# Kernel optimization log

Hardware: AMD Instinct MI355X
Metric: run time of the kernel (lower is better)

The kernel has to match this reference:

```python
import jax, jax.numpy as jnp
import numpy as np

N = 50000      # nodes
E = 600000     # edges
F_ATOM = 78
D = 128        # hidden_dim = heads * head_dim
H = 8
C = D // H     # 16
ED = 12        # edge_dim
L = 4          # num_layers
B = 512        # graphs in batch
DFF = 4 * D
SCALE = 1.0 / float(np.sqrt(C))


def setup_inputs() -> dict:
    key = jax.random.key(0)
    ks = iter(jax.random.split(key, 128))
    rn = lambda s, sc=0.05: jax.random.normal(next(ks), s, jnp.float32) * sc
    inp = {
        "x": jax.random.normal(next(ks), (N, F_ATOM), jnp.float32),
        "edge_attr": jax.random.normal(next(ks), (E, ED), jnp.float32),
        "edge_index": jax.random.randint(next(ks), (2, E), 0, N),
        "batch": jnp.sort(jax.random.randint(next(ks), (N,), 0, B)),
        "Wemb": rn((F_ATOM, D)), "bemb": jnp.zeros((D,), jnp.float32),
        "Wout": rn((D, D)), "bout": jnp.zeros((D,), jnp.float32),
    }
    def stk(s, sc=0.05):
        return jnp.stack([rn(s, sc) for _ in range(L)])
    inp.update(
        Wq=stk((D, D)), bq=jnp.zeros((L, D), jnp.float32),
        Wk=stk((D, D)), bk=jnp.zeros((L, D), jnp.float32),
        Wv=stk((D, D)), bv=jnp.zeros((L, D), jnp.float32),
        We=stk((ED, D)), be=jnp.zeros((L, D), jnp.float32),
        Wskip=stk((D, D)), bskip=jnp.zeros((L, D), jnp.float32),
        Wbeta=stk((3 * D,)),
        g1=jnp.ones((L, D), jnp.float32), b1=jnp.zeros((L, D), jnp.float32),
        g2=jnp.ones((L, D), jnp.float32), b2=jnp.zeros((L, D), jnp.float32),
        Wf1=stk((D, DFF)), bf1=jnp.zeros((L, DFF), jnp.float32),
        Wf2=stk((DFF, D)), bf2=jnp.zeros((L, D), jnp.float32),
    )
    return inp


def _ln(x, g, b):
    mu = jnp.mean(x, -1, keepdims=True)
    var = jnp.mean((x - mu) ** 2, -1, keepdims=True)
    return (x - mu) * jax.lax.rsqrt(var + 1e-5) * g + b


def _seg_softmax(alpha, dst):
    # alpha: [E, H]; softmax over edges sharing a destination node
    m = jax.ops.segment_max(alpha, dst, num_segments=N)
    m = jnp.where(jnp.isfinite(m), m, 0.0)
    ex = jnp.exp(alpha - m[dst])
    den = jax.ops.segment_sum(ex, dst, num_segments=N)
    return ex / (den[dst] + 1e-16)


def _forward(x, edge_attr, Wemb, bemb, Wq, bq, Wk, bk, Wv, bv, We, be,
             Wskip, bskip, Wbeta, g1, b1, g2, b2, Wf1, bf1, Wf2, bf2,
             Wout, bout, edge_index, batch):
    src, dst = edge_index[0], edge_index[1]
    h = x @ Wemb + bemb                                    # [N, D]
    for l in range(L):
        q = (h @ Wq[l] + bq[l]).reshape(N, H, C)
        k = (h @ Wk[l] + bk[l]).reshape(N, H, C)
        v = (h @ Wv[l] + bv[l]).reshape(N, H, C)
        e = (edge_attr @ We[l] + be[l]).reshape(E, H, C)
        kj = k[src] + e                                    # [E, H, C]
        alpha = jnp.einsum('ehc,ehc->eh', q[dst], kj) * SCALE
        a = _seg_softmax(alpha, dst)                       # [E, H]
        msg = (v[src] + e) * a[:, :, None]                 # [E, H, C]
        agg = jax.ops.segment_sum(msg, dst, num_segments=N).reshape(N, D)
        xr = h @ Wskip[l] + bskip[l]                       # root/skip transform
        beta = jax.nn.sigmoid(
            jnp.concatenate([agg, xr, agg - xr], -1) @ Wbeta[l])[:, None]
        hc = beta * xr + (1.0 - beta) * agg                # beta gate
        h = _ln(hc + h, g1[l], b1[l])
        ff = jax.nn.relu(h @ Wf1[l] + bf1[l]) @ Wf2[l] + bf2[l]
        h = _ln(ff + h, g2[l], b2[l])
    cnt = jax.ops.segment_sum(jnp.ones((N,), h.dtype), batch, num_segments=B)
    pooled = jax.ops.segment_sum(h, batch, num_segments=B) / jnp.maximum(cnt, 1.0)[:, None]
    return pooled @ Wout + bout                            # [B, D]


def reference(x, edge_attr, edge_index, batch, Wemb, bemb, Wout, bout,
              Wq, bq, Wk, bk, Wv, bv, We, be, Wskip, bskip, Wbeta,
              g1, b1, g2, b2, Wf1, bf1, Wf2, bf2):
    return _forward(x, edge_attr, Wemb, bemb, Wq, bq, Wk, bk, Wv, bv, We, be,
                    Wskip, bskip, Wbeta, g1, b1, g2, b2, Wf1, bf1, Wf2, bf2,
                    Wout, bout, edge_index, batch)
```

## Files before the change

kernel.cpp:

```cpp
#include <hip/hip_runtime.h>
#include <math.h>

#define N_NODES 50000
#define N_EDGES 600000
#define FATOM   78
#define DIM     128
#define HEADS   8
#define EDIM    12
#define LAYERS  4
#define NBATCH  512
#define NDFF    512
#define ASCALE  0.25f

typedef __attribute__((ext_vector_type(8))) short bf16x8;
typedef __attribute__((ext_vector_type(4))) float f32x4;

__device__ __forceinline__ float sum16(float v){
  #pragma unroll
  for (int m=1;m<16;m<<=1) v += __shfl_xor(v, m);
  return v;
}
__device__ __forceinline__ short f2b(float f){
  unsigned int u = __builtin_bit_cast(unsigned int, f);
  u += 0x7fffu + ((u>>16)&1u);
  return (short)(u>>16);
}
__device__ __forceinline__ float b2f_lo(unsigned int u){ return __builtin_bit_cast(float, u<<16); }
__device__ __forceinline__ float b2f_hi(unsigned int u){ return __builtin_bit_cast(float, u & 0xffff0000u); }

__device__ __forceinline__ void gload16(const short* g, short* l){
  __builtin_amdgcn_global_load_lds(
      (const __attribute__((address_space(1))) void*)g,
      (__attribute__((address_space(3))) void*)l, 16, 0, 0);
}

__global__ void count_kernel(const int* __restrict__ ei, int* __restrict__ cnt){
  int e = blockIdx.x*256 + threadIdx.x;
  if (e < N_EDGES) atomicAdd(&cnt[ei[N_EDGES + e]], 1);
}

__global__ __launch_bounds__(1024) void scan1(const int* __restrict__ cnt,
                                              int* __restrict__ row_start, int* __restrict__ bsum){
  __shared__ int lds[1024];
  int gid = blockIdx.x*1024 + threadIdx.x;
  int v = (gid < N_NODES) ? cnt[gid] : 0;
  lds[threadIdx.x] = v; __syncthreads();
  for (int off=1; off<1024; off<<=1){
    int add = (threadIdx.x>=off)?lds[threadIdx.x-off]:0;
    __syncthreads();
    lds[threadIdx.x]+=add;
    __syncthreads();
  }
  if (gid < N_NODES) row_start[gid+1] = lds[threadIdx.x];
  if (threadIdx.x==1023) bsum[blockIdx.x] = lds[1023];
}
__global__ void scan2(int* __restrict__ bsum, int nb){
  int tid = threadIdx.x;
  int v = (tid < nb) ? bsum[tid] : 0;
  #pragma unroll
  for (int off=1; off<64; off<<=1){
    int u = __shfl_up(v, off);
    if (tid >= off) v += u;
  }
  if (tid < nb) bsum[tid] = v;
}
__global__ void scan3(int* __restrict__ row_start, const int* __restrict__ bsum){
  int gid = blockIdx.x*256 + threadIdx.x;
  if (gid == 0) row_start[0] = 0;
  if (gid < N_NODES){
    int blk = gid >> 10;
    if (blk > 0) row_start[gid+1] += bsum[blk-1];
  }
}

__global__ void scatter_kernel(const int* __restrict__ ei, const float* __restrict__ ea,
                               int* __restrict__ cnt2, const int* __restrict__ row_start,
                               int* __restrict__ src_s, short* __restrict__ ea_s){
  int e = blockIdx.x*256 + threadIdx.x;
  if (e < N_EDGES){
    int d = ei[N_EDGES + e];
    int pos = atomicAdd(&cnt2[d], 1);
    int p = row_start[d] + pos;
    src_s[p] = ei[e];
    const float* src = ea + (size_t)e*EDIM;
    unsigned int* dst = (unsigned int*)(ea_s + (size_t)p*EDIM);
    #pragma unroll
    for (int j=0;j<6;j++){
      unsigned int lo = (unsigned int)(unsigned short)f2b(src[2*j]);
      unsigned int hi = (unsigned int)(unsigned short)f2b(src[2*j+1]);
      dst[j] = lo | (hi<<16);
    }
  }
}

__global__ __launch_bounds__(256) void deg_hist(const int* __restrict__ cnt, int* __restrict__ dhist){
  __shared__ int lh[256];
  lh[threadIdx.x] = 0; __syncthreads();
  int n = blockIdx.x*256 + threadIdx.x;
  if (n < N_NODES){
    int d = cnt[n]; if (d > 255) d = 255;
    atomicAdd(&lh[d], 1);
  }
  __syncthreads();
  int c = lh[threadIdx.x];
  if (c) atomicAdd(&dhist[threadIdx.x], c);
}
__global__ __launch_bounds__(256) void deg_scan(const int* __restrict__ dhist, int* __restrict__ dstart){
  __shared__ int l[256];
  int t = threadIdx.x;
  int v = dhist[t];
  l[t] = v; __syncthreads();
  for (int off=1; off<256; off<<=1){
    int add = (t>=off)? l[t-off]:0;
    __syncthreads();
    l[t]+=add;
    __syncthreads();
  }
  dstart[t] = l[t]-v;
}
__global__ __launch_bounds__(256) void deg_place(const int* __restrict__ cnt, int* __restrict__ dcnt,
                                                 const int* __restrict__ dstart, int* __restrict__ perm){
  __shared__ int lh[256];
  __shared__ int lbase[256];
  __shared__ int lrank[256];
  int t = threadIdx.x;
  lh[t] = 0; lrank[t] = 0; __syncthreads();
  int n = blockIdx.x*256 + t;
  int d = -1;
  if (n < N_NODES){
    d = cnt[n]; if (d > 255) d = 255;
    atomicAdd(&lh[d], 1);
  }
  __syncthreads();
  int c = lh[t];
  lbase[t] = c ? atomicAdd(&dcnt[t], c) : 0;
  __syncthreads();
  if (n < N_NODES){
    int r = atomicAdd(&lrank[d], 1);
    perm[dstart[d] + lbase[d] + r] = n;
  }
}

__global__ __launch_bounds__(256) void pack_weights(
  const float* __restrict__ Wq, const float* __restrict__ Wk,
  const float* __restrict__ Wv, const float* __restrict__ Ws,
  const float* __restrict__ bq, const float* __restrict__ bk,
  const float* __restrict__ bv, const float* __restrict__ bs,
  const float* __restrict__ Wf1, const float* __restrict__ Wf2,
  short* __restrict__ wq_t, short* __restrict__ wf1_t, short* __restrict__ wf2_t,
  float* __restrict__ bqkvs)
{
  int l = blockIdx.y;
  int idx = blockIdx.x*256 + threadIdx.x;
  int sec = idx >> 16, r = idx & 65535;
  if (sec == 0){
    int n = r >> 7, k = r & 127;
    const float* W = (n<128)?Wq:(n<256)?Wk:(n<384)?Wv:Ws;
    float v = W[(size_t)l*16384 + k*128 + (n&127)];
    wq_t[(size_t)l*65536 + n*128 + k] = f2b(v);
    if (k == 0){
      const float* bb = (n<128)?bq:(n<256)?bk:(n<384)?bv:bs;
      bqkvs[l*512 + n] = bb[l*128 + (n&127)];
    }
  } else if (sec == 1){
    int n = r >> 7, k = r & 127;
    wf1_t[(size_t)l*65536 + n*128 + k] = f2b(Wf1[(size_t)l*65536 + k*512 + n]);
  } else {
    int n = r >> 9, k = r & 511;
    wf2_t[(size_t)l*65536 + n*512 + k] = f2b(Wf2[(size_t)l*65536 + k*128 + n]);
  }
}

__global__ void pack_emb(const float* __restrict__ Wemb, short* __restrict__ wemb_t){
  int idx = blockIdx.x*256 + threadIdx.x;
  int nn = idx >> 7, k = idx & 127;
  wemb_t[nn*128 + k] = (k < FATOM) ? f2b(Wemb[(size_t)k*DIM + nn]) : (short)0;
}

__global__ void cast_pad_x(const float* __restrict__ x, short* __restrict__ xb){
  int idx = blockIdx.x*256 + threadIdx.x;
  int n = idx >> 6, kp = (idx & 63)*2;
  if (n >= N_NODES) return;
  float v0 = (kp   < FATOM) ? x[(size_t)n*FATOM + kp]   : 0.f;
  float v1 = (kp+1 < FATOM) ? x[(size_t)n*FATOM + kp+1] : 0.f;
  unsigned int lo = (unsigned int)(unsigned short)f2b(v0);
  unsigned int hi = (unsigned int)(unsigned short)f2b(v1);
  *(unsigned int*)(xb + (size_t)n*128 + kp) = lo | (hi<<16);
}

__global__ __launch_bounds__(256) void gemm_k128(
    const short* __restrict__ A,
    const short* __restrict__ Bt,
    const float* __restrict__ bias,
    float* __restrict__ Cf,
    short* __restrict__ Cb,
    int Nrows, int M, int relu, int nbn)
{
  __shared__ short As[128*128];
  __shared__ short Bs[128*128];
  int tid  = threadIdx.x;
  int lane = tid & 63;
  int wave = tid >> 6;
  int wr = wave >> 1, wc = wave & 1;
  int bm = blockIdx.x * 128;
  int d  = lane & 15;
  int lr = lane >> 4;

  #pragma unroll
  for (int it=0; it<8; ++it){
    int r = wave*32 + it*4 + lr;
    int oct = (d & 8) | ((d & 7) ^ (r & 7));
    int gr = bm + r; if (gr >= Nrows) gr = Nrows-1;
    gload16(A + (size_t)gr*128 + oct*8, As + (wave*32 + it*4)*128);
  }

  for (int t=0; t<nbn; ++t){
    int bn = (blockIdx.y*nbn + t)*128;
    if (t) __syncthreads();
    #pragma unroll
    for (int it=0; it<8; ++it){
      int r = wave*32 + it*4 + lr;
      int oct = (d & 8) | ((d & 7) ^ (r & 7));
      gload16(Bt + (size_t)(bn + r)*128 + oct*8, Bs + (wave*32 + it*4)*128);
    }
    f32x4 zero = {0.f,0.f,0.f,0.f};
    f32x4 acc[4][4];
    #pragma unroll
    for (int m=0;m<4;m++)
      #pragma unroll
      for (int n=0;n<4;n++) acc[m][n] = zero;

    __syncthreads();

    #pragma unroll
    for (int ks=0; ks<4; ++ks){
      int oi = ks*4 + (lane>>4);
      bf16x8 af[4], bfv[4];
      #pragma unroll
      for (int m=0;m<4;m++){
        int row = wr*64 + m*16 + (lane&15);
        int slot = (oi&8) | ((oi&7) ^ (row&7));
        af[m] = *(const bf16x8*)(As + row*128 + slot*8);
      }
      #pragma unroll
      for (int n=0;n<4;n++){
        int col = wc*64 + n*16 + (lane&15);
        int slot = (oi&8) | ((oi&7) ^ (col&7));
        bfv[n] = *(const bf16x8*)(Bs + col*128 + slot*8);
      }
      #pragma unroll
      for (int m=0;m<4;m++)
        #pragma unroll
        for (int n=0;n<4;n++)
          acc[m][n] = __builtin_amdgcn_mfma_f32_16x16x32_bf16(af[m], bfv[n], acc[m][n], 0, 0, 0);
    }

    #pragma unroll
    for (int m=0;m<4;m++){
      #pragma unroll
      for (int n=0;n<4;n++){
        int col = bn + wc*64 + n*16 + (lane&15);
        float bval = bias[col];
        #pragma unroll
        for (int j=0;j<4;j++){
          int row = bm + wr*64 + m*16 + (lane>>4)*4 + j;
          if (row < Nrows){
            float v = acc[m][n][j] + bval;
            if (relu) v = fmaxf(v, 0.f);
            if (Cf) Cf[(size_t)row*M + col] = v;
            if (Cb) Cb[(size_t)row*M + col] = f2b(v);
          }
        }
      }
    }
  }
}

__global__ __launch_bounds__(256) void gemm_ff2_ln(
    const short* __restrict__ A,
    const short* __restrict__ Bt,
    const float* __restrict__ bias,
    float* __restrict__ h, short* __restrict__ hb,
    const float* __restrict__ g, const float* __restrict__ b,
    int Nrows)
{
  __shared__ short As[128*64];
  __shared__ short Bs[128*64];
  __shared__ float red[2][128][2];
  int tid  = threadIdx.x;
  int lane = tid & 63;
  int wave = tid >> 6;
  int wr = wave >> 1, wc = wave & 1;
  int bm = blockIdx.x * 128;

  f32x4 zero = {0.f,0.f,0.f,0.f};
  f32x4 acc[4][4];
  #pragma unroll
  for (int m=0;m<4;m++)
    #pragma unroll
    for (int n=0;n<4;n++) acc[m][n] = zero;

  int r0 = wave*32;
  for (int k0 = 0; k0 < 512; k0 += 64){
    #pragma unroll
    for (int it=0; it<4; ++it){
      int rr = r0 + it*8;
      int r  = rr + (lane>>3);
      int oct = (lane&7) ^ (r&7);
      int gr = bm + r; if (gr >= Nrows) gr = Nrows-1;
      gload16(A  + (size_t)gr*512 + k0 + oct*8, As + rr*64);
      gload16(Bt + (size_t)r*512  + k0 + oct*8, Bs + rr*64);
    }
    __syncthreads();
    #pragma unroll
    for (int ks=0; ks<2; ++ks){
      bf16x8 af[4], bfv[4];
      #pragma unroll
      for (int m=0;m<4;m++){
        int row = wr*64 + m*16 + (lane&15);
        int oi  = ks*4 + (lane>>4);
        af[m] = *(const bf16x8*)(As + row*64 + ((oi ^ (row&7))<<3));
      }
      #pragma unroll
      for (int n=0;n<4;n++){
        int col = wc*64 + n*16 + (lane&15);
        int oi  = ks*4 + (lane>>4);
        bfv[n] = *(const bf16x8*)(Bs + col*64 + ((oi ^ (col&7))<<3));
      }
      #pragma unroll
      for (int m=0;m<4;m++)
        #pragma unroll
        for (int n=0;n<4;n++)
          acc[m][n] = __builtin_amdgcn_mfma_f32_16x16x32_bf16(af[m], bfv[n], acc[m][n], 0, 0, 0);
    }
    __syncthreads();
  }

  #pragma unroll
  for (int m=0;m<4;m++){
    #pragma unroll
    for (int n=0;n<4;n++){
      int col = wc*64 + n*16 + (lane&15);
      float bval = bias[col];
      #pragma unroll
      for (int j=0;j<4;j++){
        int row = wr*64 + m*16 + (lane>>4)*4 + j;
        int grow = bm + row; if (grow >= Nrows) grow = Nrows-1;
        acc[m][n][j] += bval + h[(size_t)grow*DIM + col];
      }
    }
  }
  #pragma unroll
  for (int m=0;m<4;m++){
    #pragma unroll
    for (int j=0;j<4;j++){
      float ps = 0.f, pq = 0.f;
      #pragma unroll
      for (int n=0;n<4;n++){ float v = acc[m][n][j]; ps += v; pq += v*v; }
      #pragma unroll
      for (int msk=1; msk<16; msk<<=1){ ps += __shfl_xor(ps, msk); pq += __shfl_xor(pq, msk); }
      if ((lane&15)==0){
        int row = wr*64 + m*16 + (lane>>4)*4 + j;
        red[wc][row][0] = ps;
        red[wc][row][1] = pq;
      }
    }
  }
  __syncthreads();
  #pragma unroll
  for (int m=0;m<4;m++){
    #pragma unroll
    for (int j=0;j<4;j++){
      int row = wr*64 + m*16 + (lane>>4)*4 + j;
      float S = red[0][row][0] + red[1][row][0];
      float Q = red[0][row][1] + red[1][row][1];
      float mu  = S*(1.f/128.f);
      float var = fmaxf(Q*(1.f/128.f) - mu*mu, 0.f);
      float rr  = rsqrtf(var + 1e-5f);
      int grow = bm + row;
      if (grow < Nrows){
        #pragma unroll
        for (int n=0;n<4;n++){
          int col = wc*64 + n*16 + (lane&15);
          float o = (acc[m][n][j]-mu)*rr*g[col] + b[col];
          h[(size_t)grow*DIM + col]  = o;
          hb[(size_t)grow*DIM + col] = f2b(o);
        }
      }
    }
  }
}

__global__ __launch_bounds__(256) void edge_attn_fused(
  const short* __restrict__ qkvx,
  const short* __restrict__ ea_s, const int* __restrict__ src_s,
  const float* __restrict__ Wel, const float* __restrict__ bel,
  const int* __restrict__ row_start, const int* __restrict__ perm,
  float* __restrict__ h, short* __restrict__ hb,
  const float* __restrict__ Wb, const float* __restrict__ g, const float* __restrict__ b)
{
  int wid = (blockIdx.x*256 + threadIdx.x) >> 4;
  if (wid >= N_NODES) return;
  int node = perm[wid];
  int ln = threadIdx.x & 15;
  int c0 = ln*8;

  const short* qrow = qkvx + (size_t)node*512;
  uint4 qu = *(const uint4*)(qrow + c0);
  float q0=b2f_lo(qu.x), q1=b2f_hi(qu.x), q2=b2f_lo(qu.y), q3=b2f_hi(qu.y);
  float q4=b2f_lo(qu.z), q5=b2f_hi(qu.z), q6=b2f_lo(qu.w), q7=b2f_hi(qu.w);

  float u[12];
  #pragma unroll
  for (int j=0;j<12;j++){
    float4 wA = *(const float4*)(Wel + j*DIM + c0);
    float4 wB = *(const float4*)(Wel + j*DIM + c0 + 4);
    float pp = q0*wA.x+q1*wA.y+q2*wA.z+q3*wA.w
             + q4*wB.x+q5*wB.y+q6*wB.z+q7*wB.w;
    u[j] = pp + __shfl_xor(pp,1);
  }
  float4 beA = *(const float4*)(bel + c0);
  float4 beB = *(const float4*)(bel + c0 + 4);
  float qbe;
  { float pp = q0*beA.x+q1*beA.y+q2*beA.z+q3*beA.w
             + q4*beB.x+q5*beB.y+q6*beB.z+q7*beB.w;
    qbe = pp + __shfl_xor(pp,1); }

  int rs = row_start[node], re = row_start[node+1];
  float den = 0.f;
  float av[8] = {0.f,0.f,0.f,0.f,0.f,0.f,0.f,0.f};
  float aEA[12] = {0.f,0.f,0.f,0.f,0.f,0.f,0.f,0.f,0.f,0.f,0.f,0.f};

  int i = rs;
  for (; i+2 <= re; i += 2){
    int s0 = src_s[i], s1 = src_s[i+1];
    const short* e0p = ea_s + (size_t)i*EDIM;
    uint2 a00 = *(const uint2*)(e0p);
    uint2 a01 = *(const uint2*)(e0p+4);
    uint2 a02 = *(const uint2*)(e0p+8);
    uint2 a10 = *(const uint2*)(e0p+12);
    uint2 a11 = *(const uint2*)(e0p+16);
    uint2 a12 = *(const uint2*)(e0p+20);
    const short* r0p = qkvx + (size_t)s0*512;
    const short* r1p = qkvx + (size_t)s1*512;
    uint4 ku0 = *(const uint4*)(r0p + 128 + c0);
    uint4 vu0 = *(const uint4*)(r0p + 256 + c0);
    uint4 ku1 = *(const uint4*)(r1p + 128 + c0);
    uint4 vu1 = *(const uint4*)(r1p + 256 + c0);

    float ea0[12], ea1[12];
    ea0[0]=b2f_lo(a00.x); ea0[1]=b2f_hi(a00.x); ea0[2]=b2f_lo(a00.y); ea0[3]=b2f_hi(a00.y);
    ea0[4]=b2f_lo(a01.x); ea0[5]=b2f_hi(a01.x); ea0[6]=b2f_lo(a01.y); ea0[7]=b2f_hi(a01.y);
    ea0[8]=b2f_lo(a02.x); ea0[9]=b2f_hi(a02.x); ea0[10]=b2f_lo(a02.y); ea0[11]=b2f_hi(a02.y);
    ea1[0]=b2f_lo(a10.x); ea1[1]=b2f_hi(a10.x); ea1[2]=b2f_lo(a10.y); ea1[3]=b2f_hi(a10.y);
    ea1[4]=b2f_lo(a11.x); ea1[5]=b2f_hi(a11.x); ea1[6]=b2f_lo(a11.y); ea1[7]=b2f_hi(a11.y);
    ea1[8]=b2f_lo(a12.x); ea1[9]=b2f_hi(a12.x); ea1[10]=b2f_lo(a12.y); ea1[11]=b2f_hi(a12.y);

    float pp0 = q0*b2f_lo(ku0.x) + q1*b2f_hi(ku0.x) + q2*b2f_lo(ku0.y) + q3*b2f_hi(ku0.y)
              + q4*b2f_lo(ku0.z) + q5*b2f_hi(ku0.z) + q6*b2f_lo(ku0.w) + q7*b2f_hi(ku0.w);
    float pp1 = q0*b2f_lo(ku1.x) + q1*b2f_hi(ku1.x) + q2*b2f_lo(ku1.y) + q3*b2f_hi(ku1.y)
              + q4*b2f_lo(ku1.z) + q5*b2f_hi(ku1.z) + q6*b2f_lo(ku1.w) + q7*b2f_hi(ku1.w);
    float al0 = pp0 + __shfl_xor(pp0,1) + qbe;
    float al1 = pp1 + __shfl_xor(pp1,1) + qbe;
    #pragma unroll
    for (int j=0;j<12;j++){ al0 += ea0[j]*u[j]; al1 += ea1[j]*u[j]; }
    float p0 = __expf(al0 * ASCALE);
    float p1 = __expf(al1 * ASCALE);
    den += p0 + p1;
    av[0] += p0*b2f_lo(vu0.x) + p1*b2f_lo(vu1.x);
    av[1] += p0*b2f_hi(vu0.x) + p1*b2f_hi(vu1.x);
    av[2] += p0*b2f_lo(vu0.y) + p1*b2f_lo(vu1.y);
    av[3] += p0*b2f_hi(vu0.y) + p1*b2f_hi(vu1.y);
    av[4] += p0*b2f_lo(vu0.z) + p1*b2f_lo(vu1.z);
    av[5] += p0*b2f_hi(vu0.z) + p1*b2f_hi(vu1.z);
    av[6] += p0*b2f_lo(vu0.w) + p1*b2f_lo(vu1.w);
    av[7] += p0*b2f_hi(vu0.w) + p1*b2f_hi(vu1.w);
    #pragma unroll
    for (int j=0;j<12;j++) aEA[j] += p0*ea0[j] + p1*ea1[j];
  }
  if (i < re){
    int s = src_s[i];
    const short* eap = ea_s + (size_t)i*EDIM;
    uint2 eu0 = *(const uint2*)(eap);
    uint2 eu1 = *(const uint2*)(eap+4);
    uint2 eu2 = *(const uint2*)(eap+8);
    float ea0[12];
    ea0[0]=b2f_lo(eu0.x); ea0[1]=b2f_hi(eu0.x); ea0[2]=b2f_lo(eu0.y); ea0[3]=b2f_hi(eu0.y);
    ea0[4]=b2f_lo(eu1.x); ea0[5]=b2f_hi(eu1.x); ea0[6]=b2f_lo(eu1.y); ea0[7]=b2f_hi(eu1.y);
    ea0[8]=b2f_lo(eu2.x); ea0[9]=b2f_hi(eu2.x); ea0[10]=b2f_lo(eu2.y); ea0[11]=b2f_hi(eu2.y);
    const short* srow = qkvx + (size_t)s*512;
    uint4 ku = *(const uint4*)(srow + 128 + c0);
    uint4 vu = *(const uint4*)(srow + 256 + c0);
    float pp = q0*b2f_lo(ku.x) + q1*b2f_hi(ku.x) + q2*b2f_lo(ku.y) + q3*b2f_hi(ku.y)
             + q4*b2f_lo(ku.z) + q5*b2f_hi(ku.z) + q6*b2f_lo(ku.w) + q7*b2f_hi(ku.w);
    float alpha = pp + __shfl_xor(pp,1) + qbe;
    #pragma unroll
    for (int j=0;j<12;j++) alpha += ea0[j]*u[j];
    float p = __expf(alpha * ASCALE);
    den += p;
    av[0] += p*b2f_lo(vu.x); av[1] += p*b2f_hi(vu.x);
    av[2] += p*b2f_lo(vu.y); av[3] += p*b2f_hi(vu.y);
    av[4] += p*b2f_lo(vu.z); av[5] += p*b2f_hi(vu.z);
    av[6] += p*b2f_lo(vu.w); av[7] += p*b2f_hi(vu.w);
    #pragma unroll
    for (int j=0;j<12;j++) aEA[j] += p*ea0[j];
  }

  float inv = 1.f/(den + 1e-16f);
  float gg[8];
  #pragma unroll
  for (int c=0;c<8;c++) gg[c] = av[c]*inv;
  #pragma unroll
  for (int j=0;j<12;j++){
    float wgt = aEA[j]*inv;
    float4 wA = *(const float4*)(Wel + j*DIM + c0);
    float4 wB = *(const float4*)(Wel + j*DIM + c0 + 4);
    gg[0]+=wgt*wA.x; gg[1]+=wgt*wA.y; gg[2]+=wgt*wA.z; gg[3]+=wgt*wA.w;
    gg[4]+=wgt*wB.x; gg[5]+=wgt*wB.y; gg[6]+=wgt*wB.z; gg[7]+=wgt*wB.w;
  }
  if (re > rs){
    gg[0]+=beA.x; gg[1]+=beA.y; gg[2]+=beA.z; gg[3]+=beA.w;
    gg[4]+=beB.x; gg[5]+=beB.y; gg[6]+=beB.z; gg[7]+=beB.w;
  }

  uint4 xu = *(const uint4*)(qrow + 384 + c0);
  float x[8];
  x[0]=b2f_lo(xu.x); x[1]=b2f_hi(xu.x); x[2]=b2f_lo(xu.y); x[3]=b2f_hi(xu.y);
  x[4]=b2f_lo(xu.z); x[5]=b2f_hi(xu.z); x[6]=b2f_lo(xu.w); x[7]=b2f_hi(xu.w);
  float4 hA = *(const float4*)(h + (size_t)node*DIM + c0);
  float4 hB = *(const float4*)(h + (size_t)node*DIM + c0 + 4);
  float hv[8] = {hA.x,hA.y,hA.z,hA.w,hB.x,hB.y,hB.z,hB.w};
  float4 waA = *(const float4*)(Wb + c0),       waB = *(const float4*)(Wb + c0 + 4);
  float4 wxA = *(const float4*)(Wb + DIM + c0), wxB = *(const float4*)(Wb + DIM + c0 + 4);
  float4 wdA = *(const float4*)(Wb + 2*DIM + c0), wdB = *(const float4*)(Wb + 2*DIM + c0 + 4);
  float wa[8] = {waA.x,waA.y,waA.z,waA.w,waB.x,waB.y,waB.z,waB.w};
  float wx[8] = {wxA.x,wxA.y,wxA.z,wxA.w,wxB.x,wxB.y,wxB.z,wxB.w};
  float wd[8] = {wdA.x,wdA.y,wdA.z,wdA.w,wdB.x,wdB.y,wdB.z,wdB.w};
  float sacc = 0.f;
  #pragma unroll
  for (int c=0;c<8;c++) sacc += gg[c]*wa[c] + x[c]*wx[c] + (gg[c]-x[c])*wd[c];
  sacc = sum16(sacc);
  float beta = 1.f/(1.f + __expf(-sacc));
  float t[8], ts = 0.f;
  #pragma unroll
  for (int c=0;c<8;c++){ t[c] = beta*x[c] + (1.f-beta)*gg[c] + hv[c]; ts += t[c]; }
  float mu = sum16(ts)*(1.f/128.f);
  float vs = 0.f;
  #pragma unroll
  for (int c=0;c<8;c++){ t[c] -= mu; vs += t[c]*t[c]; }
  float var = sum16(vs)*(1.f/128.f);
  float r = rsqrtf(var + 1e-5f);
  float4 gA = *(const float4*)(g + c0), gB = *(const float4*)(g + c0 + 4);
  float4 bA = *(const float4*)(b + c0), bB = *(const float4*)(b + c0 + 4);
  float gv[8] = {gA.x,gA.y,gA.z,gA.w,gB.x,gB.y,gB.z,gB.w};
  float bv[8] = {bA.x,bA.y,bA.z,bA.w,bB.x,bB.y,bB.z,bB.w};
  float o[8];
  #pragma unroll
  for (int c=0;c<8;c++) o[c] = t[c]*r*gv[c] + bv[c];
  float4 oA = {o[0],o[1],o[2],o[3]}, oB = {o[4],o[5],o[6],o[7]};
  *(float4*)(h + (size_t)node*DIM + c0)     = oA;
  *(float4*)(h + (size_t)node*DIM + c0 + 4) = oB;
  uint4 ou;
  ou.x = (unsigned int)(unsigned short)f2b(o[0]) | ((unsigned int)(unsigned short)f2b(o[1])<<16);
  ou.y = (unsigned int)(unsigned short)f2b(o[2]) | ((unsigned int)(unsigned short)f2b(o[3])<<16);
  ou.z = (unsigned int)(unsigned short)f2b(o[4]) | ((unsigned int)(unsigned short)f2b(o[5])<<16);
  ou.w = (unsigned int)(unsigned short)f2b(o[6]) | ((unsigned int)(unsigned short)f2b(o[7])<<16);
  *(uint4*)(hb + (size_t)node*DIM + c0) = ou;
}

__global__ __launch_bounds__(128) void pool_out(
  const float* __restrict__ h, const int* __restrict__ batch,
  const float* __restrict__ Wout, const float* __restrict__ bout,
  float* __restrict__ out)
{
  int bidx = blockIdx.x;
  int d = threadIdx.x;
  __shared__ int seg[2];
  __shared__ float p[DIM];
  if (d < 2){
    int target = bidx + d;
    int lo = 0, hi = N_NODES;
    while (lo < hi){ int mid = (lo+hi)>>1; if (batch[mid] < target) lo = mid+1; else hi = mid; }
    seg[d] = lo;
  }
  __syncthreads();
  int lo = seg[0], hi = seg[1];
  float s = 0.f;
  for (int n=lo; n<hi; ++n) s += h[(size_t)n*DIM + d];
  float cnt = (float)(hi - lo);
  p[d] = s / fmaxf(cnt, 1.f);
  __syncthreads();
  float o = bout[d];
  #pragma unroll 8
  for (int kk=0; kk<DIM; ++kk) o += p[kk]*Wout[kk*DIM + d];
  out[bidx*DIM + d] = o;
}

extern "C" void kernel_launch(void* const* d_in, const int* in_sizes, int n_in,
                              void* d_out, int out_size, void* d_ws, size_t ws_size,
                              hipStream_t stream)
{
  const float* x     = (const float*)d_in[0];
  const float* ea    = (const float*)d_in[1];
  const int*   ei    = (const int*)d_in[2];
  const int*   batch = (const int*)d_in[3];
  const float* Wemb  = (const float*)d_in[4];
  const float* bemb  = (const float*)d_in[5];
  const float* Wout  = (const float*)d_in[6];
  const float* bout  = (const float*)d_in[7];
  const float* Wq    = (const float*)d_in[8];
  const float* bq    = (const float*)d_in[9];
  const float* Wk    = (const float*)d_in[10];
  const float* bk    = (const float*)d_in[11];
  const float* Wv    = (const float*)d_in[12];
  const float* bv    = (const float*)d_in[13];
  const float* We    = (const float*)d_in[14];
  const float* be    = (const float*)d_in[15];
  const float* Wskip = (const float*)d_in[16];
  const float* bskip = (const float*)d_in[17];
  const float* Wbeta = (const float*)d_in[18];
  const float* g1    = (const float*)d_in[19];
  const float* b1    = (const float*)d_in[20];
  const float* g2    = (const float*)d_in[21];
  const float* b2    = (const float*)d_in[22];
  const float* Wf1   = (const float*)d_in[23];
  const float* bf1   = (const float*)d_in[24];
  const float* Wf2   = (const float*)d_in[25];
  const float* bf2   = (const float*)d_in[26];
  float* out = (float*)d_out;

  float* ws     = (float*)d_ws;
  float* h      = ws;
  float* bqkvs  = h + (size_t)N_NODES*DIM;
  short* ea_s   = (short*)(bqkvs + LAYERS*512);
  short* hb     = ea_s + (size_t)N_EDGES*EDIM;
  short* region = hb + (size_t)N_NODES*DIM;
  short* xb     = region + (size_t)N_NODES*NDFF;
  short* wemb_t = xb + (size_t)N_NODES*DIM;
  short* wq_t   = wemb_t + DIM*DIM;
  short* wf1_t  = wq_t  + (size_t)LAYERS*NDFF*DIM;
  short* wf2_t  = wf1_t + (size_t)LAYERS*NDFF*DIM;
  int*   cnt       = (int*)(wf2_t + (size_t)LAYERS*NDFF*DIM);
  int*   cnt2      = cnt + N_NODES;
  int*   row_start = cnt2 + N_NODES;
  int*   bsum      = row_start + N_NODES + 1;
  int*   dhist     = bsum + 64;
  int*   dcnt      = dhist + 256;
  int*   dstart    = dcnt + 256;
  int*   node_perm = dstart + 256;
  int*   src_s     = node_perm + N_NODES;

  hipMemsetAsync(cnt,  0, N_NODES*sizeof(int), stream);
  hipMemsetAsync(cnt2, 0, N_NODES*sizeof(int), stream);
  hipMemsetAsync(dhist, 0, 512*sizeof(int), stream);

  const int NB_SCAN = (N_NODES + 1023)/1024;
  const int NB_DEG  = (N_NODES + 255)/256;
  count_kernel<<<(N_EDGES+255)/256, 256, 0, stream>>>(ei, cnt);
  scan1<<<NB_SCAN, 1024, 0, stream>>>(cnt, row_start, bsum);
  scan2<<<1, 64, 0, stream>>>(bsum, NB_SCAN);
  scan3<<<(N_NODES+255)/256, 256, 0, stream>>>(row_start, bsum);
  deg_hist<<<NB_DEG, 256, 0, stream>>>(cnt, dhist);
  deg_scan<<<1, 256, 0, stream>>>(dhist, dstart);
  deg_place<<<NB_DEG, 256, 0, stream>>>(cnt, dcnt, dstart, node_perm);
  scatter_kernel<<<(N_EDGES+255)/256, 256, 0, stream>>>(ei, ea, cnt2, row_start, src_s, ea_s);

  pack_weights<<<dim3(768, LAYERS), 256, 0, stream>>>(
      Wq, Wk, Wv, Wskip, bq, bk, bv, bskip, Wf1, Wf2, wq_t, wf1_t, wf2_t, bqkvs);
  pack_emb<<<64, 256, 0, stream>>>(Wemb, wemb_t);
  cast_pad_x<<<(N_NODES*64 + 255)/256, 256, 0, stream>>>(x, xb);

  int gM = (N_NODES + 127)/128;
  int attnBlocks = (N_NODES*16 + 255)/256;

  gemm_k128<<<dim3(gM, 1), 256, 0, stream>>>(xb, wemb_t, bemb, h, hb, N_NODES, DIM, 0, 1);

  for (int l=0; l<LAYERS; ++l){
    gemm_k128<<<dim3(gM, 2), 256, 0, stream>>>(
        hb, wq_t + (size_t)l*NDFF*DIM, bqkvs + l*512, nullptr, region,
        N_NODES, NDFF, 0, 2);

    edge_attn_fused<<<attnBlocks, 256, 0, stream>>>(
        region, ea_s, src_s, We + (size_t)l*EDIM*DIM, be + l*DIM, row_start, node_perm,
        h, hb, Wbeta + l*3*DIM, g1 + l*DIM, b1 + l*DIM);

    gemm_k128<<<dim3(gM, 2), 256, 0, stream>>>(
        hb, wf1_t + (size_t)l*NDFF*DIM, bf1 + l*NDFF, nullptr, region,
        N_NODES, NDFF, 1, 2);

    gemm_ff2_ln<<<dim3(gM, 1), 256, 0, stream>>>(
        region, wf2_t + (size_t)l*DIM*NDFF, bf2 + l*DIM, h, hb,
        g2 + l*DIM, b2 + l*DIM, N_NODES);
  }

  pool_out<<<NBATCH, 128, 0, stream>>>(h, batch, Wout, bout, out);
}
```

Before: 878.4 us.

## Fuse FFN up and down projections with LayerNorm into one kernel

Replaces the separate FF1 GEMM (writing a bf16 N×512 intermediate to global memory) and the FF2+LayerNorm GEMM with a single kernel. Each block takes 64 rows and loops over four 128-wide chunks of the hidden dimension: it computes ReLU(h·W1+b1) into shared memory and immediately accumulates that chunk times W2 into registers. This removes the global round trip of the FFN intermediate and one launch. The cost is a smaller row tile, W2 fragments read straight from global/L2 without staging, and more shared memory per block. The attention kernel also now walks the degree-sorted node permutation in reverse order, likely to start the highest-degree nodes first for better load balance.

```diff
diff --git a/kernel.cpp b/kernel.cpp
--- a/kernel.cpp
+++ b/kernel.cpp
@@ -234,17 +234,17 @@
 
     #pragma unroll
     for (int ks=0; ks<4; ++ks){
-      int oi = ks*4 + (lane>>4);
+      int oi = ks*4 + lr;
       bf16x8 af[4], bfv[4];
       #pragma unroll
       for (int m=0;m<4;m++){
-        int row = wr*64 + m*16 + (lane&15);
+        int row = wr*64 + m*16 + d;
         int slot = (oi&8) | ((oi&7) ^ (row&7));
         af[m] = *(const bf16x8*)(As + row*128 + slot*8);
       }
       #pragma unroll
       for (int n=0;n<4;n++){
-        int col = wc*64 + n*16 + (lane&15);
+        int col = wc*64 + n*16 + d;
         int slot = (oi&8) | ((oi&7) ^ (col&7));
         bfv[n] = *(const bf16x8*)(Bs + col*128 + slot*8);
       }
@@ -259,11 +259,11 @@
     for (int m=0;m<4;m++){
       #pragma unroll
       for (int n=0;n<4;n++){
-        int col = bn + wc*64 + n*16 + (lane&15);
+        int col = bn + wc*64 + n*16 + d;
         float bval = bias[col];
         #pragma unroll
         for (int j=0;j<4;j++){
-          int row = bm + wr*64 + m*16 + (lane>>4)*4 + j;
+          int row = bm + wr*64 + m*16 + lr*4 + j;
           if (row < Nrows){
             float v = acc[m][n][j] + bval;
             if (relu) v = fmaxf(v, 0.f);
@@ -276,91 +276,149 @@
   }
 }
 
-__global__ __launch_bounds__(256) void gemm_ff2_ln(
+__global__ __launch_bounds__(256) void gemm_ffn_ln(
     const short* __restrict__ A,
-    const short* __restrict__ Bt,
-    const float* __restrict__ bias,
+    const short* __restrict__ W1t,
+    const short* __restrict__ W2t,
+    const float* __restrict__ bias1,
+    const float* __restrict__ bias2,
     float* __restrict__ h, short* __restrict__ hb,
     const float* __restrict__ g, const float* __restrict__ b,
     int Nrows)
 {
-  __shared__ short As[128*64];
-  __shared__ short Bs[128*64];
-  __shared__ float red[2][128][2];
+  __shared__ short As[64*128];
+  __shared__ short Bs[128*128];
+  __shared__ short F1[64*128];
+  __shared__ float red[2][64][2];
   int tid  = threadIdx.x;
   int lane = tid & 63;
   int wave = tid >> 6;
   int wr = wave >> 1, wc = wave & 1;
-  int bm = blockIdx.x * 128;
+  int bm = blockIdx.x * 64;
+  int d  = lane & 15;
+  int lr = lane >> 4;
+
+  #pragma unroll
+  for (int it=0; it<4; ++it){
+    int rbase = wave*16 + it*4;
+    int r = rbase + lr;
+    int oct = (d & 8) | ((d & 7) ^ (r & 7));
+    int gr = bm + r; if (gr >= Nrows) gr = Nrows-1;
+    gload16(A + (size_t)gr*128 + oct*8, As + rbase*128);
+  }
 
   f32x4 zero = {0.f,0.f,0.f,0.f};
-  f32x4 acc[4][4];
-  #pragma unroll
-  for (int m=0;m<4;m++)
-    #pragma unroll
-    for (int n=0;n<4;n++) acc[m][n] = zero;
-
-  int r0 = wave*32;
-  for (int k0 = 0; k0 < 512; k0 += 64){
-    #pragma unroll
-    for (int it=0; it<4; ++it){
-      int rr = r0 + it*8;
-      int r  = rr + (lane>>3);
-      int oct = (lane&7) ^ (r&7);
-      int gr = bm + r; if (gr >= Nrows) gr = Nrows-1;
-      gload16(A  + (size_t)gr*512 + k0 + oct*8, As + rr*64);
-      gload16(Bt + (size_t)r*512  + k0 + oct*8, Bs + rr*64);
+  f32x4 acc2[2][4];
+  #pragma unroll
+  for (int m=0;m<2;m++)
+    #pragma unroll
+    for (int n=0;n<4;n++) acc2[m][n] = zero;
+
+  for (int t=0; t<4; ++t){
+    #pragma unroll
+    for (int it=0; it<8; ++it){
+      int rbase = wave*32 + it*4;
+      int r = rbase + lr;
+      int oct = (d & 8) | ((d & 7) ^ (r & 7));
+      gload16(W1t + (size_t)(t*128 + r)*128 + oct*8, Bs + rbase*128);
     }
     __syncthreads();
-    #pragma unroll
-    for (int ks=0; ks<2; ++ks){
-      bf16x8 af[4], bfv[4];
-      #pragma unroll
-      for (int m=0;m<4;m++){
-        int row = wr*64 + m*16 + (lane&15);
-        int oi  = ks*4 + (lane>>4);
-        af[m] = *(const bf16x8*)(As + row*64 + ((oi ^ (row&7))<<3));
+
+    f32x4 acc1[2][4];
+    #pragma unroll
+    for (int m=0;m<2;m++)
+      #pragma unroll
+      for (int n=0;n<4;n++) acc1[m][n] = zero;
+    #pragma unroll
+    for (int ks=0; ks<4; ++ks){
+      int oi = ks*4 + lr;
+      bf16x8 af[2], bfv[4];
+      #pragma unroll
+      for (int m=0;m<2;m++){
+        int row = wr*32 + m*16 + d;
+        int slot = (oi&8) | ((oi&7) ^ (row&7));
+        af[m] = *(const bf16x8*)(As + row*128 + slot*8);
       }
       #pragma unroll
       for (int n=0;n<4;n++){
-        int col = wc*64 + n*16 + (lane&15);
-        int oi  = ks*4 + (lane>>4);
-        bfv[n] = *(const bf16x8*)(Bs + col*64 + ((oi ^ (col&7))<<3));
-      }
-      #pragma unroll
-      for (int m=0;m<4;m++)
+        int cn = wc*64 + n*16 + d;
+        int slot = (oi&8) | ((oi&7) ^ (cn&7));
+        bfv[n] = *(const bf16x8*)(Bs + cn*128 + slot*8);
+      }
+      #pragma unroll
+      for (int m=0;m<2;m++)
         #pragma unroll
         for (int n=0;n<4;n++)
-          acc[m][n] = __builtin_amdgcn_mfma_f32_16x16x32_bf16(af[m], bfv[n], acc[m][n], 0, 0, 0);
+          acc1[m][n] = __builtin_amdgcn_mfma_f32_16x16x32_bf16(af[m], bfv[n], acc1[m][n], 0, 0, 0);
     }
     __syncthreads();
-  }
-
-  #pragma unroll
-  for (int m=0;m<4;m++){
+
+    #pragma unroll
+    for (int m=0;m<2;m++){
+      #pragma unroll
+      for (int n=0;n<4;n++){
+        int col = wc*64 + n*16 + d;
+        float bv1 = bias1[t*128 + col];
+        int oct2 = col >> 3, within = col & 7;
+        #pragma unroll
+        for (int j=0;j<4;j++){
+          int row = wr*32 + m*16 + lr*4 + j;
+          float v = fmaxf(acc1[m][n][j] + bv1, 0.f);
+          int so = (oct2 & 8) | ((oct2 & 7) ^ (row & 7));
+          F1[row*128 + so*8 + within] = f2b(v);
+        }
+      }
+    }
+    __syncthreads();
+
+    #pragma unroll
+    for (int ks=0; ks<4; ++ks){
+      int oi = ks*4 + lr;
+      bf16x8 af[2], bfv[4];
+      #pragma unroll
+      for (int m=0;m<2;m++){
+        int row = wr*32 + m*16 + d;
+        int slot = (oi&8) | ((oi&7) ^ (row&7));
+        af[m] = *(const bf16x8*)(F1 + row*128 + slot*8);
+      }
+      #pragma unroll
+      for (int n=0;n<4;n++){
+        int col = wc*64 + n*16 + d;
+        bfv[n] = *(const bf16x8*)(W2t + (size_t)col*512 + t*128 + oi*8);
+      }
+      #pragma unroll
+      for (int m=0;m<2;m++)
+        #pragma unroll
+        for (int n=0;n<4;n++)
+          acc2[m][n] = __builtin_amdgcn_mfma_f32_16x16x32_bf16(af[m], bfv[n], acc2[m][n], 0, 0, 0);
+    }
+  }
+
+  #pragma unroll
+  for (int m=0;m<2;m++){
     #pragma unroll
     for (int n=0;n<4;n++){
-      int col = wc*64 + n*16 + (lane&15);
-      float bval = bias[col];
+      int col = wc*64 + n*16 + d;
+      float bval = bias2[col];
       #pragma unroll
       for (int j=0;j<4;j++){
-        int row = wr*64 + m*16 + (lane>>4)*4 + j;
+        int row = wr*32 + m*16 + lr*4 + j;
         int grow = bm + row; if (grow >= Nrows) grow = Nrows-1;
-        acc[m][n][j] += bval + h[(size_t)grow*DIM + col];
-      }
-    }
-  }
-  #pragma unroll
-  for (int m=0;m<4;m++){
+        acc2[m][n][j] += bval + h[(size_t)grow*DIM + col];
+      }
+    }
+  }
+  #pragma unroll
+  for (int m=0;m<2;m++){
     #pragma unroll
     for (int j=0;j<4;j++){
       float ps = 0.f, pq = 0.f;
       #pragma unroll
-      for (int n=0;n<4;n++){ float v = acc[m][n][j]; ps += v; pq += v*v; }
+      for (int n=0;n<4;n++){ float v = acc2[m][n][j]; ps += v; pq += v*v; }
       #pragma unroll
       for (int msk=1; msk<16; msk<<=1){ ps += __shfl_xor(ps, msk); pq += __shfl_xor(pq, msk); }
-      if ((lane&15)==0){
-        int row = wr*64 + m*16 + (lane>>4)*4 + j;
+      if (d == 0){
+        int row = wr*32 + m*16 + lr*4 + j;
         red[wc][row][0] = ps;
         red[wc][row][1] = pq;
       }
@@ -368,10 +426,10 @@
   }
   __syncthreads();
   #pragma unroll
-  for (int m=0;m<4;m++){
+  for (int m=0;m<2;m++){
     #pragma unroll
     for (int j=0;j<4;j++){
-      int row = wr*64 + m*16 + (lane>>4)*4 + j;
+      int row = wr*32 + m*16 + lr*4 + j;
       float S = red[0][row][0] + red[1][row][0];
       float Q = red[0][row][1] + red[1][row][1];
       float mu  = S*(1.f/128.f);
@@ -381,8 +439,8 @@
       if (grow < Nrows){
         #pragma unroll
         for (int n=0;n<4;n++){
-          int col = wc*64 + n*16 + (lane&15);
-          float o = (acc[m][n][j]-mu)*rr*g[col] + b[col];
+          int col = wc*64 + n*16 + d;
+          float o = (acc2[m][n][j]-mu)*rr*g[col] + b[col];
           h[(size_t)grow*DIM + col]  = o;
           hb[(size_t)grow*DIM + col] = f2b(o);
         }
@@ -401,7 +459,7 @@
 {
   int wid = (blockIdx.x*256 + threadIdx.x) >> 4;
   if (wid >= N_NODES) return;
-  int node = perm[wid];
+  int node = perm[N_NODES - 1 - wid];
   int ln = threadIdx.x & 15;
   int c0 = ln*8;
 
@@ -670,7 +728,8 @@
   pack_emb<<<64, 256, 0, stream>>>(Wemb, wemb_t);
   cast_pad_x<<<(N_NODES*64 + 255)/256, 256, 0, stream>>>(x, xb);
 
-  int gM = (N_NODES + 127)/128;
+  int gM  = (N_NODES + 127)/128;
+  int gM64 = (N_NODES + 63)/64;
   int attnBlocks = (N_NODES*16 + 255)/256;
 
   gemm_k128<<<dim3(gM, 1), 256, 0, stream>>>(xb, wemb_t, bemb, h, hb, N_NODES, DIM, 0, 1);
@@ -684,12 +743,9 @@
         region, ea_s, src_s, We + (size_t)l*EDIM*DIM, be + l*DIM, row_start, node_perm,
         h, hb, Wbeta + l*3*DIM, g1 + l*DIM, b1 + l*DIM);
 
-    gemm_k128<<<dim3(gM, 2), 256, 0, stream>>>(
-        hb, wf1_t + (size_t)l*NDFF*DIM, bf1 + l*NDFF, nullptr, region,
-        N_NODES, NDFF, 1, 2);
-
-    gemm_ff2_ln<<<dim3(gM, 1), 256, 0, stream>>>(
-        region, wf2_t + (size_t)l*DIM*NDFF, bf2 + l*DIM, h, hb,
+    gemm_ffn_ln<<<dim3(gM64, 1), 256, 0, stream>>>(
+        hb, wf1_t + (size_t)l*NDFF*DIM, wf2_t + (size_t)l*DIM*NDFF,
+        bf1 + l*NDFF, bf2 + l*DIM, h, hb,
         g2 + l*DIM, b2 + l*DIM, N_NODES);
   }
 
```

Result: faster. 849.2 us (-3.3%).
